# Kernel tuning notes

Measured on AMD Instinct MI355X. Metric: run time of the kernel, lower is better.

Reference implementation:

```python
import jax, jax.numpy as jnp
import numpy as np

NUM_CQ = 16
NUM_CODES = 8192
NUM_SAMPLES = 16
TEMP = 1.0
NHEADS = 4
DM = 32
EMB = 768
B, L = 64, 512


def setup_inputs():
    key = jax.random.key(0)
    ks = jax.random.split(key, 16)

    def lin(k, shape):
        fan_in = shape[-1]
        return (jax.random.uniform(k, shape, jnp.float32, -1.0, 1.0) / np.sqrt(fan_in)).astype(jnp.float32)

    xcq = jax.random.normal(ks[0], (B, L, EMB), jnp.float32)
    attn_mask = jax.random.randint(ks[1], (B, L - NUM_CQ), 0, 2, dtype=jnp.int32)
    cb = jax.random.normal(ks[2], (NUM_CODES, EMB), jnp.float32)
    codebook = 100.0 * cb / jnp.linalg.norm(cb, axis=-1, keepdims=True)  # matches 100*normalize init
    return dict(
        xcq=xcq, attn_mask=attn_mask,
        fc_in_w=lin(ks[3], (DM, EMB)), fc_in_b=jnp.zeros((DM,), jnp.float32),
        fc_out_w=lin(ks[4], (EMB, DM)), fc_out_b=jnp.zeros((EMB,), jnp.float32),
        enc_in_w=lin(ks[5], (2, 3 * DM, DM)), enc_in_b=jnp.zeros((2, 3 * DM), jnp.float32),
        enc_out_w=lin(ks[6], (2, DM, DM)), enc_out_b=jnp.zeros((2, DM), jnp.float32),
        enc_ff1_w=lin(ks[7], (2, 2 * DM, DM)), enc_ff1_b=jnp.zeros((2, 2 * DM), jnp.float32),
        enc_ff2_w=lin(ks[8], (2, DM, 2 * DM)), enc_ff2_b=jnp.zeros((2, DM), jnp.float32),
        enc_ln1_g=jnp.ones((2, DM), jnp.float32), enc_ln1_b=jnp.zeros((2, DM), jnp.float32),
        enc_ln2_g=jnp.ones((2, DM), jnp.float32), enc_ln2_b=jnp.zeros((2, DM), jnp.float32),
        codebook=codebook,
    )


def _layernorm(x, g, b):
    mu = jnp.mean(x, -1, keepdims=True)
    var = jnp.mean((x - mu) ** 2, -1, keepdims=True)
    return g * (x - mu) / jnp.sqrt(var + 1e-5) + b


def _forward(xcq, attn_mask, fc_in_w, fc_in_b, fc_out_w, fc_out_b,
             enc_in_w, enc_in_b, enc_out_w, enc_out_b,
             enc_ff1_w, enc_ff1_b, enc_ff2_w, enc_ff2_b,
             enc_ln1_g, enc_ln1_b, enc_ln2_g, enc_ln2_b, codebook):
    Bb, Ll, _ = xcq.shape
    dh = DM // NHEADS
    x = xcq @ fc_in_w.T + fc_in_b  # [B, L, 32]
    # ones for the cq tokens, then the provided mask; True = valid key
    valid = jnp.concatenate([jnp.ones((Bb, NUM_CQ), bool), attn_mask.astype(bool)], axis=1)  # [B, L]
    for l in range(2):  # torch post-norm TransformerEncoderLayer, relu, dropout=0 (eval)
        qkv = x @ enc_in_w[l].T + enc_in_b[l]
        q, k, v = jnp.split(qkv, 3, axis=-1)
        sh = lambda t: t.reshape(Bb, Ll, NHEADS, dh).transpose(0, 2, 1, 3)  # [B,h,L,dh]
        q, k, v = sh(q), sh(k), sh(v)
        scores = jnp.einsum('bhqd,bhkd->bhqk', q, k) / np.sqrt(dh)
        scores = jnp.where(valid[:, None, None, :], scores, -1e9)  # key padding mask
        attn = jax.nn.softmax(scores, axis=-1)
        o = jnp.einsum('bhqk,bhkd->bhqd', attn, v).transpose(0, 2, 1, 3).reshape(Bb, Ll, DM)
        o = o @ enc_out_w[l].T + enc_out_b[l]
        x = _layernorm(x + o, enc_ln1_g[l], enc_ln1_b[l])
        h = jax.nn.relu(x @ enc_ff1_w[l].T + enc_ff1_b[l]) @ enc_ff2_w[l].T + enc_ff2_b[l]
        x = _layernorm(x + h, enc_ln2_g[l], enc_ln2_b[l])
    xc_out = x[:, :NUM_CQ] @ fc_out_w.T + fc_out_b  # [B, ncq, 768]
    flat = xc_out.reshape(-1, EMB)  # [N, 768]
    dists = (jnp.sum(flat ** 2, 1, keepdims=True) + jnp.sum(codebook ** 2, 1)
             - 2.0 * (flat @ codebook.T))  # [N, K] squared euclidean
    logits = (-dists - 1e-5) / TEMP
    N = Bb * NUM_CQ
    # multinomial(total_count=NUM_SAMPLES): draw S categoricals per row and count
    draws = jax.random.categorical(jax.random.key(42), logits, shape=(NUM_SAMPLES, N))  # [S, N]
    rows = jnp.broadcast_to(jnp.arange(N), (NUM_SAMPLES, N))
    samples = jnp.zeros((N, NUM_CODES), jnp.float32).at[rows, draws].add(1.0)  # [N, K] counts
    xq = (samples @ codebook).reshape(xc_out.shape) / NUM_SAMPLES
    xc_quantized = xc_out + jax.lax.stop_gradient(xq - xc_out)  # straight-through estimator
    return xc_quantized


def reference(xcq, attn_mask, fc_in_w, fc_in_b, fc_out_w, fc_out_b,
              enc_in_w, enc_in_b, enc_out_w, enc_out_b,
              enc_ff1_w, enc_ff1_b, enc_ff2_w, enc_ff2_b,
              enc_ln1_g, enc_ln1_b, enc_ln2_g, enc_ln2_b, codebook):
    xc_quantized = _forward(xcq, attn_mask, fc_in_w, fc_in_b, fc_out_w, fc_out_b,
                            enc_in_w, enc_in_b, enc_out_w, enc_out_b,
                            enc_ff1_w, enc_ff1_b, enc_ff2_w, enc_ff2_b,
                            enc_ln1_g, enc_ln1_b, enc_ln2_g, enc_ln2_b, codebook)
    return (xc_quantized, xcq)
```

## Files before the change

kernel.cpp:

```cpp
#include <hip/hip_runtime.h>
#include <stdint.h>

#define NCODES 8192
#define NROWS 1024

#define OFF_LOGITS 0ll
#define OFF_X      8388608ll
#define OFF_QKV    9437184ll
#define OFF_ATTN   12582912ll
#define OFF_FLAT   13631488ll
#define OFF_CSQ    14418944ll

__device__ __forceinline__ uint32_t rotl32(uint32_t x, int r) { return (x << r) | (x >> (32 - r)); }

__device__ __forceinline__ void tf2x32_key42(uint32_t x0, uint32_t x1, uint32_t& o0, uint32_t& o1) {
  const uint32_t k0 = 0u, k1 = 42u;
  const uint32_t k2 = k0 ^ k1 ^ 0x1BD11BDAu;
  x0 += k0; x1 += k1;
  x0 += x1; x1 = rotl32(x1,13); x1 ^= x0;
  x0 += x1; x1 = rotl32(x1,15); x1 ^= x0;
  x0 += x1; x1 = rotl32(x1,26); x1 ^= x0;
  x0 += x1; x1 = rotl32(x1, 6); x1 ^= x0;
  x0 += k1; x1 += k2 + 1u;
  x0 += x1; x1 = rotl32(x1,17); x1 ^= x0;
  x0 += x1; x1 = rotl32(x1,29); x1 ^= x0;
  x0 += x1; x1 = rotl32(x1,16); x1 ^= x0;
  x0 += x1; x1 = rotl32(x1,24); x1 ^= x0;
  x0 += k2; x1 += k0 + 2u;
  x0 += x1; x1 = rotl32(x1,13); x1 ^= x0;
  x0 += x1; x1 = rotl32(x1,15); x1 ^= x0;
  x0 += x1; x1 = rotl32(x1,26); x1 ^= x0;
  x0 += x1; x1 = rotl32(x1, 6); x1 ^= x0;
  x0 += k0; x1 += k1 + 3u;
  x0 += x1; x1 = rotl32(x1,17); x1 ^= x0;
  x0 += x1; x1 = rotl32(x1,29); x1 ^= x0;
  x0 += x1; x1 = rotl32(x1,16); x1 ^= x0;
  x0 += x1; x1 = rotl32(x1,24); x1 ^= x0;
  x0 += k1; x1 += k2 + 4u;
  x0 += x1; x1 = rotl32(x1,13); x1 ^= x0;
  x0 += x1; x1 = rotl32(x1,15); x1 ^= x0;
  x0 += x1; x1 = rotl32(x1,26); x1 ^= x0;
  x0 += x1; x1 = rotl32(x1, 6); x1 ^= x0;
  x0 += k2; x1 += k0 + 5u;
  o0 = x0; o1 = x1;
}

__device__ __forceinline__ float gumbel_at(uint32_t idx) {
  uint32_t y0, y1;
  tf2x32_key42(0u, idx, y0, y1);
  uint32_t bits = y0 ^ y1;
  float f = __uint_as_float((bits >> 9) | 0x3f800000u) - 1.0f;
  float u = fmaxf(f, 1.17549435e-38f);
  return -logf(-logf(u));
}

__global__ __launch_bounds__(256) void k_fcin(const float* __restrict__ xcq,
                                              const float* __restrict__ W,
                                              const float* __restrict__ b,
                                              float* __restrict__ x,
                                              float* __restrict__ outcopy) {
  __shared__ __align__(16) float xs[2][64 * 128];
  int t = threadIdx.x;
  int w = t >> 6, lane = t & 63;
  int wu = __builtin_amdgcn_readfirstlane(w);
  long tb = (long)blockIdx.x * 64;
  const float4* W4 = (const float4*)W;
  float4* out4 = (float4*)outcopy;
  float acc[8];
  #pragma unroll
  for (int i = 0; i < 8; i++) acc[i] = 0.f;

#define STAGE(kt, buf)                                                               \
  { _Pragma("unroll")                                                                \
    for (int q = 0; q < 8; q++) {                                                    \
      int p = (w * 8 + q) * 64 + lane;                                               \
      int row = p >> 5, sl = p & 31;                                                 \
      int sls = (sl & ~7) | ((sl & 7) ^ (row & 7));                                  \
      const float* g = xcq + ((tb + row) * 192 + (kt) * 32 + sls) * 4;               \
      __builtin_amdgcn_global_load_lds(                                              \
          (const __attribute__((address_space(1))) uint32_t*)g,                      \
          (__attribute__((address_space(3))) uint32_t*)&xs[buf][p * 4], 16, 0, 0);   \
    } }

#define COMPUTE(kt, buf)                                                             \
  { _Pragma("unroll")                                                                \
    for (int j4 = 0; j4 < 32; j4++) {                                                \
      int ph = (j4 & ~7) | ((j4 & 7) ^ (lane & 7));                                  \
      float4 xv = *(const float4*)(&xs[buf][(lane * 32 + ph) * 4]);                  \
      _Pragma("unroll")                                                              \
      for (int ci = 0; ci < 8; ci++) {                                               \
        float4 wv = W4[(wu * 8 + ci) * 192 + (kt) * 32 + j4];            \
        acc[ci] += xv.x * wv.x + xv.y * wv.y + xv.z * wv.z + xv.w * wv.w;            \
      } } }

#define COPYOUT(kt, buf)                                                             \
  { int row = t >> 2, g0 = (t & 3) * 8;                                              \
    _Pragma("unroll")                                                                \
    for (int i = 0; i < 8; i++) {                                                    \
      int ph = g0 + (i ^ (row & 7));                                                 \
      float4 v = *(const float4*)(&xs[buf][(row * 32 + ph) * 4]);                    \
      out4[(tb + row) * 192 + (kt) * 32 + g0 + i] = v;                               \
    } }

#define WAITV(N) asm volatile("s_waitcnt vmcnt(" #N ")" ::: "memory")
#define CFENCE() asm volatile("" ::: "memory")
#define BAR() __builtin_amdgcn_s_barrier()

  STAGE(0, 0);
  STAGE(1, 1); WAITV(8);  BAR(); COMPUTE(0, 0); COPYOUT(0, 0); CFENCE(); BAR();
  STAGE(2, 0); WAITV(16); BAR(); COMPUTE(1, 1); COPYOUT(1, 1); CFENCE(); BAR();
  STAGE(3, 1); WAITV(16); BAR(); COMPUTE(2, 0); COPYOUT(2, 0); CFENCE(); BAR();
  STAGE(4, 0); WAITV(16); BAR(); COMPUTE(3, 1); COPYOUT(3, 1); CFENCE(); BAR();
  STAGE(5, 1); WAITV(16); BAR(); COMPUTE(4, 0); COPYOUT(4, 0); CFENCE(); BAR();
               WAITV(8);  BAR(); COMPUTE(5, 1); COPYOUT(5, 1); CFENCE();
#undef STAGE
#undef COMPUTE
#undef COPYOUT
#undef WAITV
#undef CFENCE
#undef BAR
  __syncthreads();
  float* xsf = xs[0];
  *(float4*)(xsf + lane * 36 + w * 8)     = make_float4(acc[0] + b[w*8+0], acc[1] + b[w*8+1], acc[2] + b[w*8+2], acc[3] + b[w*8+3]);
  *(float4*)(xsf + lane * 36 + w * 8 + 4) = make_float4(acc[4] + b[w*8+4], acc[5] + b[w*8+5], acc[6] + b[w*8+6], acc[7] + b[w*8+7]);
  __syncthreads();
  float4* x4 = (float4*)x;
  #pragma unroll
  for (int p = 0; p < 2; p++) {
    int f = t + 256 * p;
    int row = f >> 3, c4 = f & 7;
    x4[(tb + row) * 8 + c4] = *(const float4*)(xsf + row * 36 + c4 * 4);
  }
}

__global__ __launch_bounds__(64) void k_qkv(const float* __restrict__ x,
                                            const float* __restrict__ W,
                                            const float* __restrict__ b,
                                            float* __restrict__ qkv) {
  long token = (long)blockIdx.x * 64 + threadIdx.x;
  const float4* x4 = (const float4*)x;
  const float4* W4 = (const float4*)W;
  float4* q4 = (float4*)qkv;
  float4 xr[8];
  #pragma unroll
  for (int j4 = 0; j4 < 8; j4++) xr[j4] = x4[token * 8 + j4];
  #pragma unroll
  for (int c4 = 0; c4 < 24; c4++) {
    float s[4];
    #pragma unroll
    for (int q = 0; q < 4; q++) {
      int c = c4 * 4 + q;
      float acc = 0.f;
      #pragma unroll
      for (int j4 = 0; j4 < 8; j4++) {
        float4 wv = W4[c * 8 + j4];
        acc += xr[j4].x * wv.x + xr[j4].y * wv.y + xr[j4].z * wv.z + xr[j4].w * wv.w;
      }
      s[q] = acc + b[c];
    }
    q4[token * 24 + c4] = make_float4(s[0], s[1], s[2], s[3]);
  }
}

__global__ __launch_bounds__(256) void k_attn(const float* __restrict__ qkv,
                                              const int* __restrict__ amask,
                                              float* __restrict__ attno) {
  int z = blockIdx.x;
  int b = z >> 2;
  int h = z & 3;
  __shared__ float4 ks4[512 * 2];
  __shared__ float4 vs4[512 * 2];
  __shared__ float inval[512];
  int t = threadIdx.x;
  long qb4 = (long)b * 512 * 24;
  const float4* qkv4 = (const float4*)qkv;
  #pragma unroll
  for (int p = 0; p < 4; p++) {
    int f = t + 256 * p;
    int tok = f >> 1, hf = f & 1;
    ks4[f] = qkv4[qb4 + (long)tok * 24 + 8 + h * 2 + hf];
    vs4[f] = qkv4[qb4 + (long)tok * 24 + 16 + h * 2 + hf];
  }
  #pragma unroll
  for (int p = 0; p < 2; p++) {
    int l = t + 256 * p;
    inval[l] = (l < 16 || amask[b * 496 + (l - 16)] != 0) ? 0.f : 1.f;
  }
  __syncthreads();
  const float scale = 0.35355339059327373f;
  float4 qa0 = qkv4[qb4 + (long)t * 24 + h * 2];
  float4 qb0 = qkv4[qb4 + (long)t * 24 + h * 2 + 1];
  float4 qa1 = qkv4[qb4 + (long)(t + 256) * 24 + h * 2];
  float4 qb1 = qkv4[qb4 + (long)(t + 256) * 24 + h * 2 + 1];
  float m0 = -3.4e38f, m1 = -3.4e38f;
  #pragma unroll 2
  for (int lk = 0; lk < 512; lk++) {
    float4 ka = ks4[lk * 2], kb = ks4[lk * 2 + 1];
    float iv = inval[lk];
    float s0 = qa0.x*ka.x + qa0.y*ka.y + qa0.z*ka.z + qa0.w*ka.w
             + qb0.x*kb.x + qb0.y*kb.y + qb0.z*kb.z + qb0.w*kb.w;
    s0 *= scale;
    s0 = iv != 0.f ? -1e9f : s0;
    m0 = fmaxf(m0, s0);
    float s1 = qa1.x*ka.x + qa1.y*ka.y + qa1.z*ka.z + qa1.w*ka.w
             + qb1.x*kb.x + qb1.y*kb.y + qb1.z*kb.z + qb1.w*kb.w;
    s1 *= scale;
    s1 = iv != 0.f ? -1e9f : s1;
    m1 = fmaxf(m1, s1);
  }
  float d0 = 0.f, d1 = 0.f;
  float4 o00 = make_float4(0,0,0,0), o01 = make_float4(0,0,0,0);
  float4 o10 = make_float4(0,0,0,0), o11 = make_float4(0,0,0,0);
  #pragma unroll 2
  for (int lk = 0; lk < 512; lk++) {
    float4 ka = ks4[lk * 2], kb = ks4[lk * 2 + 1];
    float4 va = vs4[lk * 2], vb = vs4[lk * 2 + 1];
    float iv = inval[lk];
    float s0 = qa0.x*ka.x + qa0.y*ka.y + qa0.z*ka.z + qa0.w*ka.w
             + qb0.x*kb.x + qb0.y*kb.y + qb0.z*kb.z + qb0.w*kb.w;
    s0 *= scale;
    s0 = iv != 0.f ? -1e9f : s0;
    float p0 = expf(s0 - m0);
    d0 += p0;
    o00.x += p0 * va.x; o00.y += p0 * va.y; o00.z += p0 * va.z; o00.w += p0 * va.w;
    o01.x += p0 * vb.x; o01.y += p0 * vb.y; o01.z += p0 * vb.z; o01.w += p0 * vb.w;
    float s1 = qa1.x*ka.x + qa1.y*ka.y + qa1.z*ka.z + qa1.w*ka.w
             + qb1.x*kb.x + qb1.y*kb.y + qb1.z*kb.z + qb1.w*kb.w;
    s1 *= scale;
    s1 = iv != 0.f ? -1e9f : s1;
    float p1 = expf(s1 - m1);
    d1 += p1;
    o10.x += p1 * va.x; o10.y += p1 * va.y; o10.z += p1 * va.z; o10.w += p1 * va.w;
    o11.x += p1 * vb.x; o11.y += p1 * vb.y; o11.z += p1 * vb.z; o11.w += p1 * vb.w;
  }
  float4* a4 = (float4*)attno;
  float inv0 = 1.f / d0;
  long ob0 = ((long)b * 512 + t) * 8 + h * 2;
  a4[ob0]     = make_float4(o00.x*inv0, o00.y*inv0, o00.z*inv0, o00.w*inv0);
  a4[ob0 + 1] = make_float4(o01.x*inv0, o01.y*inv0, o01.z*inv0, o01.w*inv0);
  float inv1 = 1.f / d1;
  long ob1 = ((long)b * 512 + t + 256) * 8 + h * 2;
  a4[ob1]     = make_float4(o10.x*inv1, o10.y*inv1, o10.z*inv1, o10.w*inv1);
  a4[ob1 + 1] = make_float4(o11.x*inv1, o11.y*inv1, o11.z*inv1, o11.w*inv1);
}

__global__ __launch_bounds__(64) void k_oproj_ln(const float* __restrict__ attno,
                                                 const float* __restrict__ W,
                                                 const float* __restrict__ b,
                                                 const float* __restrict__ g,
                                                 const float* __restrict__ beta,
                                                 float* __restrict__ x) {
  long token = (long)blockIdx.x * 64 + threadIdx.x;
  const float4* a4 = (const float4*)attno;
  const float4* x4 = (const float4*)x;
  const float4* W4 = (const float4*)W;
  float4 orow[8];
  float xr[32];
  #pragma unroll
  for (int j4 = 0; j4 < 8; j4++) {
    orow[j4] = a4[token * 8 + j4];
    float4 v = x4[token * 8 + j4];
    xr[j4*4] = v.x; xr[j4*4+1] = v.y; xr[j4*4+2] = v.z; xr[j4*4+3] = v.w;
  }
  float v[32];
  #pragma unroll
  for (int c = 0; c < 32; c++) {
    float acc = 0.f;
    #pragma unroll
    for (int j4 = 0; j4 < 8; j4++) {
      float4 wv = W4[c * 8 + j4];
      acc += orow[j4].x * wv.x + orow[j4].y * wv.y + orow[j4].z * wv.z + orow[j4].w * wv.w;
    }
    v[c] = acc + b[c] + xr[c];
  }
  float mu = 0.f;
  #pragma unroll
  for (int c = 0; c < 32; c++) mu += v[c];
  mu *= 0.03125f;
  float var = 0.f;
  #pragma unroll
  for (int c = 0; c < 32; c++) { float d = v[c] - mu; var += d * d; }
  var *= 0.03125f;
  float inv = 1.f / sqrtf(var + 1e-5f);
  float4* xo4 = (float4*)x;
  #pragma unroll
  for (int j4 = 0; j4 < 8; j4++) {
    float4 o;
    o.x = g[j4*4]   * (v[j4*4]   - mu) * inv + beta[j4*4];
    o.y = g[j4*4+1] * (v[j4*4+1] - mu) * inv + beta[j4*4+1];
    o.z = g[j4*4+2] * (v[j4*4+2] - mu) * inv + beta[j4*4+2];
    o.w = g[j4*4+3] * (v[j4*4+3] - mu) * inv + beta[j4*4+3];
    xo4[token * 8 + j4] = o;
  }
}

__global__ __launch_bounds__(64) void k_ffn_ln(const float* __restrict__ x,
                                               const float* __restrict__ W1,
                                               const float* __restrict__ b1,
                                               const float* __restrict__ W2,
                                               const float* __restrict__ b2,
                                               const float* __restrict__ g,
                                               const float* __restrict__ beta,
                                               float* __restrict__ xout) {
  long token = (long)blockIdx.x * 64 + threadIdx.x;
  const float4* x4 = (const float4*)x;
  const float4* W14 = (const float4*)W1;
  const float4* W24 = (const float4*)W2;
  float xr[32];
  #pragma unroll
  for (int j4 = 0; j4 < 8; j4++) {
    float4 v = x4[token * 8 + j4];
    xr[j4*4] = v.x; xr[j4*4+1] = v.y; xr[j4*4+2] = v.z; xr[j4*4+3] = v.w;
  }
  float h[64];
  #pragma unroll
  for (int c = 0; c < 64; c++) {
    float acc = 0.f;
    #pragma unroll
    for (int j4 = 0; j4 < 8; j4++) {
      float4 wv = W14[c * 8 + j4];
      acc += xr[j4*4] * wv.x + xr[j4*4+1] * wv.y + xr[j4*4+2] * wv.z + xr[j4*4+3] * wv.w;
    }
    h[c] = fmaxf(acc + b1[c], 0.f);
  }
  float v[32];
  #pragma unroll
  for (int c = 0; c < 32; c++) {
    float acc = 0.f;
    #pragma unroll
    for (int j4 = 0; j4 < 16; j4++) {
      float4 wv = W24[c * 16 + j4];
      acc += h[j4*4] * wv.x + h[j4*4+1] * wv.y + h[j4*4+2] * wv.z + h[j4*4+3] * wv.w;
    }
    v[c] = acc + b2[c] + xr[c];
  }
  float mu = 0.f;
  #pragma unroll
  for (int c = 0; c < 32; c++) mu += v[c];
  mu *= 0.03125f;
  float var = 0.f;
  #pragma unroll
  for (int c = 0; c < 32; c++) { float d = v[c] - mu; var += d * d; }
  var *= 0.03125f;
  float inv = 1.f / sqrtf(var + 1e-5f);
  float4* xo4 = (float4*)xout;
  #pragma unroll
  for (int j4 = 0; j4 < 8; j4++) {
    float4 o;
    o.x = g[j4*4]   * (v[j4*4]   - mu) * inv + beta[j4*4];
    o.y = g[j4*4+1] * (v[j4*4+1] - mu) * inv + beta[j4*4+1];
    o.z = g[j4*4+2] * (v[j4*4+2] - mu) * inv + beta[j4*4+2];
    o.w = g[j4*4+3] * (v[j4*4+3] - mu) * inv + beta[j4*4+3];
    xo4[token * 8 + j4] = o;
  }
}

__global__ __launch_bounds__(256) void k_fcout(const float* __restrict__ x,
                                               const float* __restrict__ W,
                                               const float* __restrict__ b,
                                               float* __restrict__ flat) {
  int bb = blockIdx.x;
  __shared__ float xs[16 * 32];
  int t = threadIdx.x;
  if (t < 128) {
    int row = t >> 3, j4 = t & 7;
    *(float4*)(xs + row * 32 + j4 * 4) =
        *(const float4*)(x + ((long)bb * 512 + row) * 32 + j4 * 4);
  }
  __syncthreads();
  #pragma unroll
  for (int i = 0; i < 3; i++) {
    int e = t + 256 * i;
    const float4* w4 = (const float4*)(W + e * 32);
    float4 wv[8];
    #pragma unroll
    for (int j4 = 0; j4 < 8; j4++) wv[j4] = w4[j4];
    float bias = b[e];
    #pragma unroll
    for (int r = 0; r < 16; r++) {
      float s = 0.f;
      #pragma unroll
      for (int j4 = 0; j4 < 8; j4++) {
        const float* xr = xs + r * 32 + j4 * 4;
        s += xr[0] * wv[j4].x + xr[1] * wv[j4].y + xr[2] * wv[j4].z + xr[3] * wv[j4].w;
      }
      flat[((long)bb * 16 + r) * 768 + e] = s + bias;
    }
  }
}

__global__ __launch_bounds__(256) void k_cbsq(const float* __restrict__ cb,
                                              float* __restrict__ cb_sq) {
  int w = threadIdx.x >> 6, lane = threadIdx.x & 63;
  int k = blockIdx.x * 4 + w;
  const float* row = cb + (long)k * 768;
  float s = 0.f;
  #pragma unroll
  for (int i = 0; i < 12; i++) { float v = row[lane + 64 * i]; s += v * v; }
  #pragma unroll
  for (int off = 32; off >= 1; off >>= 1) s += __shfl_xor(s, off);
  if (lane == 0) cb_sq[k] = s;
}

__device__ __forceinline__ ushort f2bf(float x) {
  uint32_t u = __float_as_uint(x);
  uint32_t r = (u + 0x7fffu + ((u >> 16) & 1u)) >> 16;
  return (ushort)r;
}

__global__ __launch_bounds__(256) void k_tobf16(const float* __restrict__ src,
                                                ushort* __restrict__ dst, long n4) {
  long i = (long)blockIdx.x * 256 + threadIdx.x;
  if (i >= n4) return;
  float4 v = ((const float4*)src)[i];
  ushort4 o;
  o.x = f2bf(v.x); o.y = f2bf(v.y); o.z = f2bf(v.z); o.w = f2bf(v.w);
  ((ushort4*)dst)[i] = o;
}

typedef __attribute__((ext_vector_type(8))) short bf16x8;
typedef __attribute__((ext_vector_type(4))) float f32x4;

__global__ __launch_bounds__(256, 2) void k_logits_mfma(const ushort* __restrict__ fbf,
                                                        const ushort* __restrict__ cbbf,
                                                        float* __restrict__ approx) {
  __shared__ __align__(16) short As[128 * 64];
  __shared__ __align__(16) short Bs[128 * 64];
  int t = threadIdx.x;
  int mb = blockIdx.x & 7;
  int nb = blockIdx.x >> 3;
  int w = t >> 6, lane = t & 63;
  int wr = w >> 1, wc = w & 1;

  f32x4 zero; zero.x = 0.f; zero.y = 0.f; zero.z = 0.f; zero.w = 0.f;
  f32x4 acc[4][4];
  #pragma unroll
  for (int i = 0; i < 4; i++)
    #pragma unroll
    for (int j = 0; j < 4; j++) acc[i][j] = zero;

  for (int kt = 0; kt < 12; kt++) {
    int kc = kt * 64;
    bf16x8 ra[4], rb[4];
    #pragma unroll
    for (int p = 0; p < 4; p++) {
      int li = p * 256 + t;
      int row = li >> 3, s = li & 7;
      ra[p] = *(const bf16x8*)(fbf + (long)(mb * 128 + row) * 768 + kc + s * 8);
      rb[p] = *(const bf16x8*)(cbbf + (long)(nb * 128 + row) * 768 + kc + s * 8);
    }
    __syncthreads();
    #pragma unroll
    for (int p = 0; p < 4; p++) {
      int li = p * 256 + t;
      int row = li >> 3, s = li & 7, ss = s ^ (row & 7);
      *(bf16x8*)(As + row * 64 + ss * 8) = ra[p];
      *(bf16x8*)(Bs + row * 64 + ss * 8) = rb[p];
    }
    __syncthreads();
    #pragma unroll
    for (int ks = 0; ks < 2; ks++) {
      int slot = ks * 4 + (lane >> 4);
      bf16x8 a[4], b[4];
      #pragma unroll
      for (int i = 0; i < 4; i++) {
        int rowa = wr * 64 + i * 16 + (lane & 15);
        a[i] = *(const bf16x8*)(As + rowa * 64 + (slot ^ (rowa & 7)) * 8);
        int rowb = wc * 64 + i * 16 + (lane & 15);
        b[i] = *(const bf16x8*)(Bs + rowb * 64 + (slot ^ (rowb & 7)) * 8);
      }
      #pragma unroll
      for (int i = 0; i < 4; i++)
        #pragma unroll
        for (int j = 0; j < 4; j++)
          acc[i][j] = __builtin_amdgcn_mfma_f32_16x16x32_bf16(a[i], b[j], acc[i][j], 0, 0, 0);
    }
  }
  long rbase = (long)mb * 128 + wr * 64 + (lane >> 4) * 4;
  int cbase = nb * 128 + wc * 64 + (lane & 15);
  #pragma unroll
  for (int i = 0; i < 4; i++) {
    #pragma unroll
    for (int j = 0; j < 4; j++) {
      f32x4 v = acc[i][j];
      long r0 = rbase + i * 16;
      int c = cbase + j * 16;
      approx[(r0 + 0) * 8192 + c] = 2.f * v.x;
      approx[(r0 + 1) * 8192 + c] = 2.f * v.y;
      approx[(r0 + 2) * 8192 + c] = 2.f * v.z;
      approx[(r0 + 3) * 8192 + c] = 2.f * v.w;
    }
  }
}

__global__ __launch_bounds__(256) void k_sample(const float* __restrict__ approx,
                                                const float* __restrict__ cb,
                                                const float* __restrict__ csq,
                                                const float* __restrict__ flat,
                                                float* __restrict__ out0) {
  int n = blockIdx.x, t = threadIdx.x;
  const float* arow = approx + (long)n * 8192;
  __shared__ float s_max[4];
  __shared__ int s_cnt;
  __shared__ int cand[8192];
  __shared__ float fs[768];
  __shared__ float redv[64];
  __shared__ int redi[64];
  __shared__ int draws[16];
  if (t < 192) ((float4*)fs)[t] = ((const float4*)(flat + (long)n * 768))[t];
  float va[32];
  float m = -3.4e38f;
  #pragma unroll
  for (int i = 0; i < 32; i++) { va[i] = arow[t + 256 * i]; m = fmaxf(m, va[i]); }
  #pragma unroll
  for (int off = 32; off >= 1; off >>= 1) m = fmaxf(m, __shfl_xor(m, off));
  if ((t & 63) == 0) s_max[t >> 6] = m;
  if (t == 0) s_cnt = 0;
  __syncthreads();
  float rowmax = fmaxf(fmaxf(s_max[0], s_max[1]), fmaxf(s_max[2], s_max[3]));
  float thresh = rowmax - 30.0f;
  #pragma unroll
  for (int i = 0; i < 32; i++) {
    if (va[i] >= thresh) { int p = atomicAdd(&s_cnt, 1); cand[p] = t + 256 * i; }
  }
  __syncthreads();
  int ncand = s_cnt;
  float bv[16]; int bi[16];
  #pragma unroll
  for (int s = 0; s < 16; s++) { bv[s] = -3.4e38f; bi[s] = 0x7fffffff; }
  for (int c = t; c < ncand; c += 256) {
    int k = cand[c];
    const float4* cb4 = (const float4*)(cb + (long)k * 768);
    float acc = 0.f;
    #pragma unroll 8
    for (int j4 = 0; j4 < 192; j4++) {
      float4 wv = cb4[j4];
      const float* xr = fs + j4 * 4;
      acc = fmaf(xr[0], wv.x, acc);
      acc = fmaf(xr[1], wv.y, acc);
      acc = fmaf(xr[2], wv.z, acc);
      acc = fmaf(xr[3], wv.w, acc);
    }
    float lg = 2.f * acc - csq[k] - 1e-5f;
    #pragma unroll
    for (int s = 0; s < 16; s++) {
      uint32_t idx = ((uint32_t)((s << 10) + n) << 13) | (uint32_t)k;
      float val = gumbel_at(idx) + lg;
      if (val > bv[s] || (val == bv[s] && k < bi[s])) { bv[s] = val; bi[s] = k; }
    }
  }
  #pragma unroll
  for (int s = 0; s < 16; s++) {
    #pragma unroll
    for (int off = 32; off >= 1; off >>= 1) {
      float ov = __shfl_xor(bv[s], off);
      int oi = __shfl_xor(bi[s], off);
      if (ov > bv[s] || (ov == bv[s] && oi < bi[s])) { bv[s] = ov; bi[s] = oi; }
    }
    if ((t & 63) == 0) { redv[s * 4 + (t >> 6)] = bv[s]; redi[s * 4 + (t >> 6)] = bi[s]; }
  }
  __syncthreads();
  if (t < 16) {
    float bvv = redv[t * 4]; int bii = redi[t * 4];
    #pragma unroll
    for (int w = 1; w < 4; w++) {
      float ov = redv[t * 4 + w]; int oi = redi[t * 4 + w];
      if (ov > bvv || (ov == bvv && oi < bii)) { bvv = ov; bii = oi; }
    }
    draws[t] = bii;
  }
  __syncthreads();
  #pragma unroll
  for (int i = 0; i < 3; i++) {
    int e = t + 256 * i;
    float ssum = 0.f;
    #pragma unroll
    for (int s = 0; s < 16; s++) ssum += cb[(long)draws[s] * 768 + e];
    float xq = ssum * 0.0625f;
    float fl = fs[e];
    out0[(long)n * 768 + e] = fl + (xq - fl);
  }
}

extern "C" void kernel_launch(void* const* d_in, const int* in_sizes, int n_in,
                              void* d_out, int out_size, void* d_ws, size_t ws_size,
                              hipStream_t stream) {
  (void)in_sizes; (void)n_in; (void)out_size; (void)ws_size;
  const float* xcq      = (const float*)d_in[0];
  const int*   amask    = (const int*)d_in[1];
  const float* fc_in_w  = (const float*)d_in[2];
  const float* fc_in_b  = (const float*)d_in[3];
  const float* fc_out_w = (const float*)d_in[4];
  const float* fc_out_b = (const float*)d_in[5];
  const float* enc_in_w = (const float*)d_in[6];
  const float* enc_in_b = (const float*)d_in[7];
  const float* enc_out_w= (const float*)d_in[8];
  const float* enc_out_b= (const float*)d_in[9];
  const float* ff1w     = (const float*)d_in[10];
  const float* ff1b     = (const float*)d_in[11];
  const float* ff2w     = (const float*)d_in[12];
  const float* ff2b     = (const float*)d_in[13];
  const float* ln1g     = (const float*)d_in[14];
  const float* ln1b     = (const float*)d_in[15];
  const float* ln2g     = (const float*)d_in[16];
  const float* ln2b     = (const float*)d_in[17];
  const float* cb       = (const float*)d_in[18];
  float* out = (float*)d_out;
  float* ws  = (float*)d_ws;

  float* x      = ws + OFF_X;
  float* qkv    = ws + OFF_QKV;
  float* attno  = ws + OFF_ATTN;
  float* flat   = ws + OFF_FLAT;
  float* csq    = ws + OFF_CSQ;
  float* approx = ws + OFF_LOGITS;
  ushort* cbbf  = (ushort*)(ws + OFF_QKV);
  ushort* fbf   = (ushort*)(ws + OFF_ATTN);

  k_fcin<<<512, 256, 0, stream>>>(xcq, fc_in_w, fc_in_b, x, out + 786432);
  for (int l = 0; l < 2; l++) {
    k_qkv<<<512, 64, 0, stream>>>(x, enc_in_w + l * 96 * 32, enc_in_b + l * 96, qkv);
    k_attn<<<256, 256, 0, stream>>>(qkv, amask, attno);
    k_oproj_ln<<<512, 64, 0, stream>>>(attno, enc_out_w + l * 32 * 32, enc_out_b + l * 32,
                                       ln1g + l * 32, ln1b + l * 32, x);
    k_ffn_ln<<<512, 64, 0, stream>>>(x, ff1w + l * 64 * 32, ff1b + l * 64,
                                     ff2w + l * 32 * 64, ff2b + l * 32,
                                     ln2g + l * 32, ln2b + l * 32, x);
  }
  k_fcout<<<64, 256, 0, stream>>>(x, fc_out_w, fc_out_b, flat);
  k_cbsq<<<2048, 256, 0, stream>>>(cb, csq);
  k_tobf16<<<6144, 256, 0, stream>>>(cb, cbbf, 1572864ll);
  k_tobf16<<<768, 256, 0, stream>>>(flat, fbf, 196608ll);
  k_logits_mfma<<<512, 256, 0, stream>>>(fbf, cbbf, approx);
  k_sample<<<1024, 256, 0, stream>>>(approx, cb, csq, flat, out);
}
```

Baseline: 1.031 ms.

## Rewrite fc_in as split-K shuffle reduction and spread fc_out across more blocks

fc_in drops its LDS double-buffered async-copy pipeline. Each token is now handled by 16 lanes that each compute a slice of the K dimension for all 32 outputs, and the partial sums are combined with width-16 xor shuffles, so the kernel launches 2048 blocks instead of 512. fc_out moves from 64 blocks looping over 16 rows to one block per output row (1024 blocks), which raises parallelism for a tiny grid. The cost is more register pressure (32 accumulators), repeated weight reads from cache, and 32 five-step shuffle reductions per thread in fc_in.

```diff
diff --git a/kernel.cpp b/kernel.cpp
--- a/kernel.cpp
+++ b/kernel.cpp
@@ -54,82 +54,48 @@
   return -logf(-logf(u));
 }
 
-__global__ __launch_bounds__(256) void k_fcin(const float* __restrict__ xcq,
-                                              const float* __restrict__ W,
-                                              const float* __restrict__ b,
-                                              float* __restrict__ x,
-                                              float* __restrict__ outcopy) {
-  __shared__ __align__(16) float xs[2][64 * 128];
+__global__ __launch_bounds__(256, 4) void k_fcin(const float* __restrict__ xcq,
+                                                 const float* __restrict__ W,
+                                                 const float* __restrict__ b,
+                                                 float* __restrict__ x,
+                                                 float* __restrict__ outcopy) {
   int t = threadIdx.x;
-  int w = t >> 6, lane = t & 63;
-  int wu = __builtin_amdgcn_readfirstlane(w);
-  long tb = (long)blockIdx.x * 64;
+  int sub = t & 15;
+  long tok = (long)blockIdx.x * 16 + (t >> 4);
+  const float4* xcq4 = (const float4*)xcq;
   const float4* W4 = (const float4*)W;
   float4* out4 = (float4*)outcopy;
-  float acc[8];
-  #pragma unroll
-  for (int i = 0; i < 8; i++) acc[i] = 0.f;
-
-#define STAGE(kt, buf)                                                               \
-  { _Pragma("unroll")                                                                \
-    for (int q = 0; q < 8; q++) {                                                    \
-      int p = (w * 8 + q) * 64 + lane;                                               \
-      int row = p >> 5, sl = p & 31;                                                 \
-      int sls = (sl & ~7) | ((sl & 7) ^ (row & 7));                                  \
-      const float* g = xcq + ((tb + row) * 192 + (kt) * 32 + sls) * 4;               \
-      __builtin_amdgcn_global_load_lds(                                              \
-          (const __attribute__((address_space(1))) uint32_t*)g,                      \
-          (__attribute__((address_space(3))) uint32_t*)&xs[buf][p * 4], 16, 0, 0);   \
-    } }
-
-#define COMPUTE(kt, buf)                                                             \
-  { _Pragma("unroll")                                                                \
-    for (int j4 = 0; j4 < 32; j4++) {                                                \
-      int ph = (j4 & ~7) | ((j4 & 7) ^ (lane & 7));                                  \
-      float4 xv = *(const float4*)(&xs[buf][(lane * 32 + ph) * 4]);                  \
-      _Pragma("unroll")                                                              \
-      for (int ci = 0; ci < 8; ci++) {                                               \
-        float4 wv = W4[(wu * 8 + ci) * 192 + (kt) * 32 + j4];            \
-        acc[ci] += xv.x * wv.x + xv.y * wv.y + xv.z * wv.z + xv.w * wv.w;            \
-      } } }
-
-#define COPYOUT(kt, buf)                                                             \
-  { int row = t >> 2, g0 = (t & 3) * 8;                                              \
-    _Pragma("unroll")                                                                \
-    for (int i = 0; i < 8; i++) {                                                    \
-      int ph = g0 + (i ^ (row & 7));                                                 \
-      float4 v = *(const float4*)(&xs[buf][(row * 32 + ph) * 4]);                    \
-      out4[(tb + row) * 192 + (kt) * 32 + g0 + i] = v;                               \
-    } }
-
-#define WAITV(N) asm volatile("s_waitcnt vmcnt(" #N ")" ::: "memory")
-#define CFENCE() asm volatile("" ::: "memory")
-#define BAR() __builtin_amdgcn_s_barrier()
-
-  STAGE(0, 0);
-  STAGE(1, 1); WAITV(8);  BAR(); COMPUTE(0, 0); COPYOUT(0, 0); CFENCE(); BAR();
-  STAGE(2, 0); WAITV(16); BAR(); COMPUTE(1, 1); COPYOUT(1, 1); CFENCE(); BAR();
-  STAGE(3, 1); WAITV(16); BAR(); COMPUTE(2, 0); COPYOUT(2, 0); CFENCE(); BAR();
-  STAGE(4, 0); WAITV(16); BAR(); COMPUTE(3, 1); COPYOUT(3, 1); CFENCE(); BAR();
-  STAGE(5, 1); WAITV(16); BAR(); COMPUTE(4, 0); COPYOUT(4, 0); CFENCE(); BAR();
-               WAITV(8);  BAR(); COMPUTE(5, 1); COPYOUT(5, 1); CFENCE();
-#undef STAGE
-#undef COMPUTE
-#undef COPYOUT
-#undef WAITV
-#undef CFENCE
-#undef BAR
-  __syncthreads();
-  float* xsf = xs[0];
-  *(float4*)(xsf + lane * 36 + w * 8)     = make_float4(acc[0] + b[w*8+0], acc[1] + b[w*8+1], acc[2] + b[w*8+2], acc[3] + b[w*8+3]);
-  *(float4*)(xsf + lane * 36 + w * 8 + 4) = make_float4(acc[4] + b[w*8+4], acc[5] + b[w*8+5], acc[6] + b[w*8+6], acc[7] + b[w*8+7]);
-  __syncthreads();
+  float acc[32];
+  #pragma unroll
+  for (int c = 0; c < 32; c++) acc[c] = 0.f;
+  #pragma unroll
+  for (int i = 0; i < 12; i++) {
+    int j4 = sub + 16 * i;
+    float4 v = xcq4[tok * 192 + j4];
+    out4[tok * 192 + j4] = v;
+    #pragma unroll
+    for (int c = 0; c < 32; c++) {
+      float4 wv = W4[c * 192 + j4];
+      acc[c] += v.x * wv.x + v.y * wv.y + v.z * wv.z + v.w * wv.w;
+    }
+  }
+  #pragma unroll
+  for (int c = 0; c < 32; c++) {
+    #pragma unroll
+    for (int off = 1; off <= 8; off <<= 1)
+      acc[c] += __shfl_xor(acc[c], off, 16);
+  }
   float4* x4 = (float4*)x;
   #pragma unroll
-  for (int p = 0; p < 2; p++) {
-    int f = t + 256 * p;
-    int row = f >> 3, c4 = f & 7;
-    x4[(tb + row) * 8 + c4] = *(const float4*)(xsf + row * 36 + c4 * 4);
+  for (int s8 = 0; s8 < 8; s8++) {
+    if (sub == s8) {
+      float4 o;
+      o.x = acc[4*s8+0] + b[4*s8+0];
+      o.y = acc[4*s8+1] + b[4*s8+1];
+      o.z = acc[4*s8+2] + b[4*s8+2];
+      o.w = acc[4*s8+3] + b[4*s8+3];
+      x4[tok * 8 + s8] = o;
+    }
   }
 }
 
@@ -359,33 +325,25 @@
                                                const float* __restrict__ W,
                                                const float* __restrict__ b,
                                                float* __restrict__ flat) {
-  int bb = blockIdx.x;
-  __shared__ float xs[16 * 32];
+  int n = blockIdx.x;
+  int bb = n >> 4, r = n & 15;
+  long xrow = (long)bb * 512 + r;
+  const float4* x4 = (const float4*)x;
+  float4 xr[8];
+  #pragma unroll
+  for (int j4 = 0; j4 < 8; j4++) xr[j4] = x4[xrow * 8 + j4];
   int t = threadIdx.x;
-  if (t < 128) {
-    int row = t >> 3, j4 = t & 7;
-    *(float4*)(xs + row * 32 + j4 * 4) =
-        *(const float4*)(x + ((long)bb * 512 + row) * 32 + j4 * 4);
-  }
-  __syncthreads();
   #pragma unroll
   for (int i = 0; i < 3; i++) {
     int e = t + 256 * i;
     const float4* w4 = (const float4*)(W + e * 32);
-    float4 wv[8];
-    #pragma unroll
-    for (int j4 = 0; j4 < 8; j4++) wv[j4] = w4[j4];
-    float bias = b[e];
-    #pragma unroll
-    for (int r = 0; r < 16; r++) {
-      float s = 0.f;
-      #pragma unroll
-      for (int j4 = 0; j4 < 8; j4++) {
-        const float* xr = xs + r * 32 + j4 * 4;
-        s += xr[0] * wv[j4].x + xr[1] * wv[j4].y + xr[2] * wv[j4].z + xr[3] * wv[j4].w;
-      }
-      flat[((long)bb * 16 + r) * 768 + e] = s + bias;
-    }
+    float s = 0.f;
+    #pragma unroll
+    for (int j4 = 0; j4 < 8; j4++) {
+      float4 wv = w4[j4];
+      s += xr[j4].x * wv.x + xr[j4].y * wv.y + xr[j4].z * wv.z + xr[j4].w * wv.w;
+    }
+    flat[(long)n * 768 + e] = s + b[e];
   }
 }
 
@@ -617,7 +575,7 @@
   ushort* cbbf  = (ushort*)(ws + OFF_QKV);
   ushort* fbf   = (ushort*)(ws + OFF_ATTN);
 
-  k_fcin<<<512, 256, 0, stream>>>(xcq, fc_in_w, fc_in_b, x, out + 786432);
+  k_fcin<<<2048, 256, 0, stream>>>(xcq, fc_in_w, fc_in_b, x, out + 786432);
   for (int l = 0; l < 2; l++) {
     k_qkv<<<512, 64, 0, stream>>>(x, enc_in_w + l * 96 * 32, enc_in_b + l * 96, qkv);
     k_attn<<<256, 256, 0, stream>>>(qkv, amask, attno);
@@ -627,7 +585,7 @@
                                      ff2w + l * 32 * 64, ff2b + l * 32,
                                      ln2g + l * 32, ln2b + l * 32, x);
   }
-  k_fcout<<<64, 256, 0, stream>>>(x, fc_out_w, fc_out_b, flat);
+  k_fcout<<<1024, 256, 0, stream>>>(x, fc_out_w, fc_out_b, flat);
   k_cbsq<<<2048, 256, 0, stream>>>(cb, csq);
   k_tobf16<<<6144, 256, 0, stream>>>(cb, cbbf, 1572864ll);
   k_tobf16<<<768, 256, 0, stream>>>(flat, fbf, 196608ll);
```

After: 1.287 ms. +24.8%, slower.
